# Kernel optimization log

Hardware: AMD Instinct MI355X
Metric: run time of the kernel (lower is better)

## Reference

```python
import jax, jax.numpy as jnp
import numpy as np

M, N = 4096, 4096

def _make_expk(n):
    k = np.arange(n, dtype=np.float64) * np.pi / (2.0 * n)
    return jnp.asarray(np.stack([np.cos(k), np.sin(k)], axis=-1), dtype=jnp.float32)

def setup_inputs() -> dict:
    key = jax.random.key(0)
    x = jax.random.normal(key, (M, N), dtype=jnp.float32)
    return {"x": x, "expkM": _make_expk(M), "expkN": _make_expk(N)}

def _idct_last(X, expk):
    """1D IDCT (inverse of unnormalized DCT-II) along last axis via Makhoul's
    N-point FFT trick. expk[k] = (cos, sin) of pi*k/(2N), i.e. e^{j pi k/(2N)}."""
    n = X.shape[-1]
    Xv = X * 0.5
    # V[k] = (Xv[k] - j*Xv[n-k]) * e^{j pi k/(2n)}, with imag part 0 at k=0
    tail = -jnp.flip(Xv, axis=-1)[..., :-1]
    Vi = jnp.concatenate([jnp.zeros_like(Xv[..., :1]), tail], axis=-1)
    W = expk[:, 0] + 1j * expk[:, 1]
    V = (Xv + 1j * Vi) * W
    v = jnp.fft.ifft(V, axis=-1).real.astype(X.dtype)
    # de-interleave: out[2m] = v[m], out[2m+1] = v[n-1-m]
    out = jnp.zeros_like(X)
    out = out.at[..., 0::2].set(v[..., : n - n // 2])
    out = out.at[..., 1::2].set(jnp.flip(v, axis=-1)[..., : n // 2])
    return out

def reference(x, expkM, expkN):
    # separable 2D IDCT: last axis (N) then first axis (M)
    y = _idct_last(x, expkN)
    y = _idct_last(y.T, expkM).T
    return y
```

## Files before the change

kernel.cpp:

```cpp
#include <hip/hip_runtime.h>
#include <math.h>


#define TT 256

constexpr float W64R[32] = {
    1.0f, 0.995184726672197f, 0.980785280403230f, 0.956940335732209f,
    0.923879532511287f, 0.881921264348355f, 0.831469612302545f, 0.773010453362737f,
    0.707106781186548f, 0.634393284163645f, 0.555570233019602f, 0.471396736825998f,
    0.382683432365090f, 0.290284677254462f, 0.195090322016128f, 0.0980171403295606f,
    0.0f, -0.0980171403295606f, -0.195090322016128f, -0.290284677254462f,
    -0.382683432365090f, -0.471396736825998f, -0.555570233019602f, -0.634393284163645f,
    -0.707106781186548f, -0.773010453362737f, -0.831469612302545f, -0.881921264348355f,
    -0.923879532511287f, -0.956940335732209f, -0.980785280403230f, -0.995184726672197f};
constexpr float W64I[32] = {
    0.0f, 0.0980171403295606f, 0.195090322016128f, 0.290284677254462f,
    0.382683432365090f, 0.471396736825998f, 0.555570233019602f, 0.634393284163645f,
    0.707106781186548f, 0.773010453362737f, 0.831469612302545f, 0.881921264348355f,
    0.923879532511287f, 0.956940335732209f, 0.980785280403230f, 0.995184726672197f,
    1.0f, 0.995184726672197f, 0.980785280403230f, 0.956940335732209f,
    0.923879532511287f, 0.881921264348355f, 0.831469612302545f, 0.773010453362737f,
    0.707106781186548f, 0.634393284163645f, 0.555570233019602f, 0.471396736825998f,
    0.382683432365090f, 0.290284677254462f, 0.195090322016128f, 0.0980171403295606f};

__device__ __forceinline__ constexpr int brev(int x, int bits) {
    int r = 0;
    for (int i = 0; i < bits; ++i) { r = (r << 1) | (x & 1); x >>= 1; }
    return r;
}

__device__ __forceinline__ float vadd(float a, float b) { return a + b; }
__device__ __forceinline__ float vsub(float a, float b) { return a - b; }
__device__ __forceinline__ float vmul(float a, float s) { return a * s; }
__device__ __forceinline__ float2 vadd(float2 a, float2 b) { return make_float2(a.x + b.x, a.y + b.y); }
__device__ __forceinline__ float2 vsub(float2 a, float2 b) { return make_float2(a.x - b.x, a.y - b.y); }
__device__ __forceinline__ float2 vmul(float2 a, float s) { return make_float2(a.x * s, a.y * s); }

template <int NP, typename V>
__device__ __forceinline__ void fft_dif(V* re, V* im) {
#pragma unroll
    for (int h = NP / 2; h >= 1; h >>= 1) {
#pragma unroll
        for (int b = 0; b < NP; b += 2 * h) {
#pragma unroll
            for (int k = 0; k < h; ++k) {
                V ur = re[b + k], ui = im[b + k];
                V vr = re[b + k + h], vi = im[b + k + h];
                V dr = vsub(ur, vr), di = vsub(ui, vi);
                re[b + k] = vadd(ur, vr);
                im[b + k] = vadd(ui, vi);
                float wr = W64R[k * (32 / h)], wi = W64I[k * (32 / h)];
                re[b + k + h] = vsub(vmul(dr, wr), vmul(di, wi));
                im[b + k + h] = vadd(vmul(dr, wi), vmul(di, wr));
            }
        }
    }
}

__global__ void tw_init_kernel(float2* __restrict__ tw2048,
                               float2* __restrict__ ca, float2* __restrict__ cb,
                               float2* __restrict__ cc, float2* __restrict__ cd) {
    int k = blockIdx.x * TT + threadIdx.x;
    const double s = 0.5 / 4096.0;
    double aw = M_PI * (double)k / 2048.0;
    double wr = cos(aw), wi = sin(aw);
    double a1 = M_PI * (double)k / 8192.0;
    double e1r = cos(a1), e1i = sin(a1);
    double a2 = M_PI * (double)(k + 2048) / 8192.0;
    double e2r = cos(a2), e2i = sin(a2);
    double Ar = s * ((1.0 - wi) * e1r - wr * e1i);
    double Ai = s * ((1.0 - wi) * e1i + wr * e1r);
    double Br = (k == 0) ? 0.0 : Ai;
    double Bi = (k == 0) ? 0.0 : -Ar;
    double Cr = s * ((1.0 + wi) * e2r + wr * e2i);
    double Ci = s * ((1.0 + wi) * e2i - wr * e2r);
    ca[k] = make_float2((float)Ar, (float)Ai);
    cb[k] = make_float2((float)Br, (float)Bi);
    cc[k] = make_float2((float)Cr, (float)Ci);
    cd[k] = make_float2((float)Ci, (float)-Cr);
    double at = M_PI * (double)k / 1024.0;
    tw2048[k] = make_float2((float)cos(at), (float)sin(at));
}

__global__ __launch_bounds__(TT, 1) void col_a_kernel(
    const float* __restrict__ x,
    const float2* __restrict__ ca, const float2* __restrict__ cb,
    const float2* __restrict__ cc, const float2* __restrict__ cd,
    const float2* __restrict__ tw2048, float2* __restrict__ T1) {
    int c = blockIdx.x * 64 + threadIdx.x;
    int k1 = blockIdx.y * 4 + threadIdx.y;
    float fr[32], fi[32];
#pragma unroll
    for (int k2 = 0; k2 < 32; ++k2) {
        int k = k1 + 64 * k2;
        float xa = x[(size_t)k * 4096 + c];
        float xb = x[(size_t)((4096 - k) & 4095) * 4096 + c];
        float xc = x[(size_t)(2048 + k) * 4096 + c];
        float xd = x[(size_t)(2048 - k) * 4096 + c];
        float2 A = ca[k], B = cb[k], C = cc[k], D = cd[k];
        fr[k2] = A.x * xa + B.x * xb + C.x * xc + D.x * xd;
        fi[k2] = A.y * xa + B.y * xb + C.y * xc + D.y * xd;
    }
    fft_dif<32, float>(fr, fi);
#pragma unroll
    for (int j = 0; j < 32; ++j) {
        int n2 = brev(j, 5);
        float2 w = tw2048[k1 * n2];
        float2 o = make_float2(fr[j] * w.x - fi[j] * w.y,
                               fr[j] * w.y + fi[j] * w.x);
        T1[(size_t)(k1 * 32 + n2) * 4096 + c] = o;
    }
}

__global__ __launch_bounds__(TT, 1) void col_b_kernel(
    const float2* __restrict__ T1, float* __restrict__ out) {
    const int t = threadIdx.x;
    const int wv = t >> 6;
    const int l = t & 63;
    const int par = l >> 5;
    const int c = blockIdx.x * 32 + (l & 31);
    const int n2 = blockIdx.y * 4 + wv;
    float fr[32], fi[32];
#pragma unroll
    for (int a = 0; a < 32; ++a) {
        int k1 = 2 * a + par;
        float2 v = T1[(size_t)(k1 * 32 + n2) * 4096 + c];
        fr[a] = v.x; fi[a] = v.y;
    }
    fft_dif<32, float>(fr, fi);
    const float sgn = par ? -1.0f : 1.0f;
#pragma unroll
    for (int j = 0; j < 32; ++j) {
        int n = brev(j, 5);
        float wr = par ? W64R[n] : 1.0f;
        float wi = par ? W64I[n] : 0.0f;
        float vr = fr[j] * wr - fi[j] * wi;
        float vi = fr[j] * wi + fi[j] * wr;
        float orr = __shfl_xor(vr, 32, 64);
        float oii = __shfl_xor(vi, 32, 64);
        float zr = orr + sgn * vr;
        float zi = oii + sgn * vi;
        int n1 = par ? (n + 32) : n;
        int m = 32 * n1 + n2;
        int r_re = (n1 < 32) ? 4 * m     : 8191 - 4 * m;
        int r_im = (n1 < 32) ? 4 * m + 2 : 8189 - 4 * m;
        out[(size_t)r_re * 4096 + c] = zr;
        out[(size_t)r_im * 4096 + c] = zi;
    }
}

#define C_SQ2 0.70710678118654752440f
__device__ __forceinline__ void radix8(const float* ar, const float* ai,
                                       float* tr, float* ti) {
    float s04r = ar[0] + ar[4], s04i = ai[0] + ai[4];
    float d04r = ar[0] - ar[4], d04i = ai[0] - ai[4];
    float s26r = ar[2] + ar[6], s26i = ai[2] + ai[6];
    float d26r = ar[2] - ar[6], d26i = ai[2] - ai[6];
    float E0r = s04r + s26r, E0i = s04i + s26i;
    float E1r = d04r - d26i, E1i = d04i + d26r;
    float E2r = s04r - s26r, E2i = s04i - s26i;
    float E3r = d04r + d26i, E3i = d04i - d26r;
    float s15r = ar[1] + ar[5], s15i = ai[1] + ai[5];
    float d15r = ar[1] - ar[5], d15i = ai[1] - ai[5];
    float s37r = ar[3] + ar[7], s37i = ai[3] + ai[7];
    float d37r = ar[3] - ar[7], d37i = ai[3] - ai[7];
    float O0r = s15r + s37r, O0i = s15i + s37i;
    float O1r = d15r - d37i, O1i = d15i + d37r;
    float O2r = s15r - s37r, O2i = s15i - s37i;
    float O3r = d15r + d37i, O3i = d15i - d37r;
    float W1r = C_SQ2 * (O1r - O1i), W1i = C_SQ2 * (O1r + O1i);
    float W2r = -O2i, W2i = O2r;
    float W3r = -C_SQ2 * (O3r + O3i), W3i = C_SQ2 * (O3r - O3i);
    tr[0] = E0r + O0r; ti[0] = E0i + O0i;
    tr[4] = E0r - O0r; ti[4] = E0i - O0i;
    tr[1] = E1r + W1r; ti[1] = E1i + W1i;
    tr[5] = E1r - W1r; ti[5] = E1i - W1i;
    tr[2] = E2r + W2r; ti[2] = E2i + W2i;
    tr[6] = E2r - W2r; ti[6] = E2i - W2i;
    tr[3] = E3r + W3r; ti[3] = E3i + W3i;
    tr[7] = E3r - W3r; ti[7] = E3i - W3i;
}

__global__ __launch_bounds__(TT) void idct_rows_kernel(
    const float2* __restrict__ ca, const float2* __restrict__ cb,
    const float2* __restrict__ cc, const float2* __restrict__ cd,
    const float2* __restrict__ tw2048, float* __restrict__ io) {
    __shared__ float pool[8576];
    float* b0r = pool;
    float* b0i = pool + 2112;
    float* b1r = pool + 4224;
    float* b1i = pool + 6400;
    float* stg = pool + 4224;
    const int t = threadIdx.x;
    float* __restrict__ xr = io + (size_t)blockIdx.x * 4096;

#pragma unroll
    for (int u = 0; u < 4; ++u) {
        int idx = t + 256 * u;
        float4 v = ((const float4*)xr)[idx];
        *(float4*)&stg[4 * idx] = v;
    }
    __syncthreads();

    float zr[8], zi[8], tr[8], ti[8];
#pragma unroll
    for (int p = 0; p < 8; ++p) {
        int k = t + 256 * p;
        float xa = stg[k];
        float xb = stg[(4096 - k) & 4095];
        float xc = stg[2048 + k];
        float xd = stg[2048 - k];
        float2 A = ca[k], B = cb[k], C = cc[k], D = cd[k];
        zr[p] = A.x * xa + B.x * xb + C.x * xc + D.x * xd;
        zi[p] = A.y * xa + B.y * xb + C.y * xc + D.y * xd;
    }
    radix8(zr, zi, tr, ti);
    {
        int baseA = 8 * t + (t >> 2);
        b0r[baseA] = tr[0]; b0i[baseA] = ti[0];
#pragma unroll
        for (int q = 1; q < 8; ++q) {
            float2 w = tw2048[(t * q) & 2047];
            b0r[baseA + q] = w.x * tr[q] - w.y * ti[q];
            b0i[baseA + q] = w.x * ti[q] + w.y * tr[q];
        }
    }
    __syncthreads();
    {
        float ar[8], ai[8];
        int rb = t + (t >> 5);
#pragma unroll
        for (int p = 0; p < 8; ++p) { ar[p] = b0r[rb + 264 * p]; ai[p] = b0i[rb + 264 * p]; }
        radix8(ar, ai, tr, ti);
        int j = t >> 3, k = t & 7, wj = 8 * j;
        int baseB = 68 * j + k;
        b1r[baseB] = tr[0]; b1i[baseB] = ti[0];
#pragma unroll
        for (int q = 1; q < 8; ++q) {
            int off = baseB + 8 * q + (q >> 1);
            float2 w = tw2048[(wj * q) & 2047];
            b1r[off] = w.x * tr[q] - w.y * ti[q];
            b1i[off] = w.x * ti[q] + w.y * tr[q];
        }
    }
    __syncthreads();
    {
        float ar[8], ai[8];
        int rb = t + (t >> 4);
#pragma unroll
        for (int p = 0; p < 8; ++p) { ar[p] = b1r[rb + 272 * p]; ai[p] = b1i[rb + 272 * p]; }
        radix8(ar, ai, tr, ti);
        int j = t >> 6, wj = 64 * j, k = t & 63;
        int baseC = 528 * j + k + (k >> 5);
        b0r[baseC] = tr[0]; b0i[baseC] = ti[0];
#pragma unroll
        for (int q = 1; q < 8; ++q) {
            int off = baseC + 66 * q;
            float2 w = tw2048[(wj * q) & 2047];
            b0r[off] = w.x * tr[q] - w.y * ti[q];
            b0i[off] = w.x * ti[q] + w.y * tr[q];
        }
    }
    __syncthreads();
#pragma unroll
    for (int u = 0; u < 2; ++u) {
        int b = t + 256 * u;
        int rb = b + (b >> 5);
        int wb = b + (b >> 4);
        float a0r = b0r[rb], a0i = b0i[rb];
        float a1r = b0r[rb + 528], a1i = b0i[rb + 528];
        float a2r = b0r[rb + 1056], a2i = b0i[rb + 1056];
        float a3r = b0r[rb + 1584], a3i = b0i[rb + 1584];
        float s02r = a0r + a2r, s02i = a0i + a2i;
        float d02r = a0r - a2r, d02i = a0i - a2i;
        float s13r = a1r + a3r, s13i = a1i + a3i;
        float d13r = a1r - a3r, d13i = a1i - a3i;
        b1r[wb] = s02r + s13r;          b1i[wb] = s02i + s13i;
        b1r[wb + 544] = d02r - d13i;    b1i[wb + 544] = d02i + d13r;
        b1r[wb + 1088] = s02r - s13r;   b1i[wb + 1088] = s02i - s13i;
        b1r[wb + 1632] = d02r + d13i;   b1i[wb + 1632] = d02i - d13r;
    }
    __syncthreads();
#pragma unroll
    for (int i = 0; i < 4; ++i) {
        int s = t + 256 * i;
        int l2 = 2047 - s;
        int ms = s + (s >> 4);
        int ml = l2 + (l2 >> 4);
        float4 o = make_float4(b1r[ms], b1i[ml], b1i[ms], b1r[ml]);
        *(float4*)&xr[4 * s] = o;
    }
}

extern "C" void kernel_launch(void* const* d_in, const int* in_sizes, int n_in,
                              void* d_out, int out_size, void* d_ws, size_t ws_size,
                              hipStream_t stream) {
    const float* x = (const float*)d_in[0];
    float* out = (float*)d_out;

    float2* tw2048 = (float2*)d_ws;
    float2* ca = (float2*)((char*)d_ws + 1 * 16384);
    float2* cb = (float2*)((char*)d_ws + 2 * 16384);
    float2* cc = (float2*)((char*)d_ws + 3 * 16384);
    float2* cd = (float2*)((char*)d_ws + 4 * 16384);
    float2* T1 = (float2*)((char*)d_ws + (1 << 20));

    tw_init_kernel<<<8, TT, 0, stream>>>(tw2048, ca, cb, cc, cd);
    col_a_kernel<<<dim3(64, 16), dim3(64, 4), 0, stream>>>(x, ca, cb, cc, cd, tw2048, T1);
    col_b_kernel<<<dim3(128, 8), TT, 0, stream>>>(T1, out);
    idct_rows_kernel<<<4096, TT, 0, stream>>>(ca, cb, cc, cd, tw2048, out);
}
```

Baseline: 195.2 us.

## Split col_a 32-point FFT across lane pairs with cross-half shuffle combine

The column pre-FFT stage now gives each 32-point FFT to two lanes that each run a 16-point FFT on even or odd inputs, then combine them with a radix-2 butterfly through __shfl_xor across the wavefront halves. This halves per-thread registers and doubles the grid, and launch_bounds no longer pins one block per CU, so occupancy can rise. The four coefficient tables are packed into one float4 table so each element needs a single load. Each warp now covers 32 columns instead of 64, which narrows coalesced rows, and the shuffles add cross-lane traffic.

```diff
diff --git a/kernel.cpp b/kernel.cpp
--- a/kernel.cpp
+++ b/kernel.cpp
@@ -32,9 +32,6 @@
 __device__ __forceinline__ float vadd(float a, float b) { return a + b; }
 __device__ __forceinline__ float vsub(float a, float b) { return a - b; }
 __device__ __forceinline__ float vmul(float a, float s) { return a * s; }
-__device__ __forceinline__ float2 vadd(float2 a, float2 b) { return make_float2(a.x + b.x, a.y + b.y); }
-__device__ __forceinline__ float2 vsub(float2 a, float2 b) { return make_float2(a.x - b.x, a.y - b.y); }
-__device__ __forceinline__ float2 vmul(float2 a, float s) { return make_float2(a.x * s, a.y * s); }
 
 template <int NP, typename V>
 __device__ __forceinline__ void fft_dif(V* re, V* im) {
@@ -59,7 +56,8 @@
 
 __global__ void tw_init_kernel(float2* __restrict__ tw2048,
                                float2* __restrict__ ca, float2* __restrict__ cb,
-                               float2* __restrict__ cc, float2* __restrict__ cd) {
+                               float2* __restrict__ cc, float2* __restrict__ cd,
+                               float4* __restrict__ cAC) {
     int k = blockIdx.x * TT + threadIdx.x;
     const double s = 0.5 / 4096.0;
     double aw = M_PI * (double)k / 2048.0;
@@ -78,36 +76,49 @@
     cb[k] = make_float2((float)Br, (float)Bi);
     cc[k] = make_float2((float)Cr, (float)Ci);
     cd[k] = make_float2((float)Ci, (float)-Cr);
+    cAC[k] = make_float4((float)Ar, (float)Ai, (float)Cr, (float)Ci);
     double at = M_PI * (double)k / 1024.0;
     tw2048[k] = make_float2((float)cos(at), (float)sin(at));
 }
 
-__global__ __launch_bounds__(TT, 1) void col_a_kernel(
-    const float* __restrict__ x,
-    const float2* __restrict__ ca, const float2* __restrict__ cb,
-    const float2* __restrict__ cc, const float2* __restrict__ cd,
+__global__ __launch_bounds__(TT) void col_a_kernel(
+    const float* __restrict__ x, const float4* __restrict__ cAC,
     const float2* __restrict__ tw2048, float2* __restrict__ T1) {
-    int c = blockIdx.x * 64 + threadIdx.x;
-    int k1 = blockIdx.y * 4 + threadIdx.y;
-    float fr[32], fi[32];
-#pragma unroll
-    for (int k2 = 0; k2 < 32; ++k2) {
+    const int l = threadIdx.x;
+    const int par = l >> 5;
+    const int c = blockIdx.x * 32 + (l & 31);
+    const int k1 = blockIdx.y * 4 + threadIdx.y;
+    float fr[16], fi[16];
+#pragma unroll
+    for (int a = 0; a < 16; ++a) {
+        int k2 = 2 * a + par;
         int k = k1 + 64 * k2;
         float xa = x[(size_t)k * 4096 + c];
         float xb = x[(size_t)((4096 - k) & 4095) * 4096 + c];
         float xc = x[(size_t)(2048 + k) * 4096 + c];
         float xd = x[(size_t)(2048 - k) * 4096 + c];
-        float2 A = ca[k], B = cb[k], C = cc[k], D = cd[k];
-        fr[k2] = A.x * xa + B.x * xb + C.x * xc + D.x * xd;
-        fi[k2] = A.y * xa + B.y * xb + C.y * xc + D.y * xd;
-    }
-    fft_dif<32, float>(fr, fi);
-#pragma unroll
-    for (int j = 0; j < 32; ++j) {
-        int n2 = brev(j, 5);
-        float2 w = tw2048[k1 * n2];
-        float2 o = make_float2(fr[j] * w.x - fi[j] * w.y,
-                               fr[j] * w.y + fi[j] * w.x);
+        float4 P = cAC[k];
+        float bs = (k == 0) ? 0.0f : 1.0f;
+        fr[a] = P.x * xa + bs * P.y * xb + P.z * xc + P.w * xd;
+        fi[a] = P.y * xa - bs * P.x * xb + P.w * xc - P.z * xd;
+    }
+    fft_dif<16, float>(fr, fi);
+    const float sgn = par ? -1.0f : 1.0f;
+#pragma unroll
+    for (int j = 0; j < 16; ++j) {
+        int n = brev(j, 4);
+        float wr = par ? W64R[2 * n] : 1.0f;
+        float wi = par ? W64I[2 * n] : 0.0f;
+        float vr = fr[j] * wr - fi[j] * wi;
+        float vi = fr[j] * wi + fi[j] * wr;
+        float orr = __shfl_xor(vr, 32, 64);
+        float oii = __shfl_xor(vi, 32, 64);
+        float zr = orr + sgn * vr;
+        float zi = oii + sgn * vi;
+        int n2 = par ? (n + 16) : n;
+        float2 w2 = tw2048[k1 * n2];
+        float2 o = make_float2(zr * w2.x - zi * w2.y,
+                               zr * w2.y + zi * w2.x);
         T1[(size_t)(k1 * 32 + n2) * 4096 + c] = o;
     }
 }
@@ -303,10 +314,11 @@
     float2* cb = (float2*)((char*)d_ws + 2 * 16384);
     float2* cc = (float2*)((char*)d_ws + 3 * 16384);
     float2* cd = (float2*)((char*)d_ws + 4 * 16384);
+    float4* cAC = (float4*)((char*)d_ws + 5 * 16384);
     float2* T1 = (float2*)((char*)d_ws + (1 << 20));
 
-    tw_init_kernel<<<8, TT, 0, stream>>>(tw2048, ca, cb, cc, cd);
-    col_a_kernel<<<dim3(64, 16), dim3(64, 4), 0, stream>>>(x, ca, cb, cc, cd, tw2048, T1);
+    tw_init_kernel<<<8, TT, 0, stream>>>(tw2048, ca, cb, cc, cd, cAC);
+    col_a_kernel<<<dim3(128, 16), dim3(64, 4), 0, stream>>>(x, cAC, tw2048, T1);
     col_b_kernel<<<dim3(128, 8), TT, 0, stream>>>(T1, out);
     idct_rows_kernel<<<4096, TT, 0, stream>>>(ca, cb, cc, cd, tw2048, out);
 }
```

New measurement: 188.4 us. -3.5%, faster.
